# Optimization experiments

Hardware: AMD Instinct MI355X
Metric: run time of the kernel (lower is better)

The kernel has to match this reference:

```python
import jax, jax.numpy as jnp
import numpy as np

N_NODES = 100000
N_EDGES = 640000
IN_DIM, HID_DIM, OUT_DIM = 128, 64, 32


def setup_inputs() -> dict:
    key = jax.random.key(0)
    ks = jax.random.split(key, 8)
    x = jax.random.normal(ks[0], (N_NODES, IN_DIM), dtype=jnp.float32)
    edge_index = jax.random.randint(ks[1], (2, N_EDGES), 0, N_NODES, dtype=jnp.int64)
    # SAGEConv params: lin_l (applied to aggregated neighbors, has bias),
    # lin_r (applied to root node, no bias) -- PyG defaults.
    s1 = 1.0 / np.sqrt(IN_DIM)
    s2 = 1.0 / np.sqrt(HID_DIM)
    W1l = jax.random.uniform(ks[2], (HID_DIM, IN_DIM), jnp.float32, -s1, s1)
    b1 = jax.random.uniform(ks[3], (HID_DIM,), jnp.float32, -s1, s1)
    W1r = jax.random.uniform(ks[4], (HID_DIM, IN_DIM), jnp.float32, -s1, s1)
    W2l = jax.random.uniform(ks[5], (OUT_DIM, HID_DIM), jnp.float32, -s2, s2)
    b2 = jax.random.uniform(ks[6], (OUT_DIM,), jnp.float32, -s2, s2)
    W2r = jax.random.uniform(ks[7], (OUT_DIM, HID_DIM), jnp.float32, -s2, s2)
    return {"x": x, "edge_index": edge_index,
            "W1l": W1l, "b1": b1, "W1r": W1r,
            "W2l": W2l, "b2": b2, "W2r": W2r}


def _sage_conv(x, src, dst, Wl, b, Wr, num_nodes):
    # mean aggregation of source features onto destination nodes
    msg = x[src]                                                # [E, d]
    agg = jax.ops.segment_sum(msg, dst, num_segments=num_nodes)  # [N, d]
    cnt = jax.ops.segment_sum(jnp.ones((src.shape[0],), x.dtype), dst,
                              num_segments=num_nodes)            # [N]
    agg = agg / jnp.maximum(cnt, 1.0)[:, None]
    # out = lin_l(mean_neighbors) + lin_r(x)
    return agg @ Wl.T + b + x @ Wr.T


def reference(x, edge_index, W1l, b1, W1r, W2l, b2, W2r):
    src, dst = edge_index[0], edge_index[1]
    n = x.shape[0]
    h = jax.nn.relu(_sage_conv(x, src, dst, W1l, b1, W1r, n))
    out = _sage_conv(h, src, dst, W2l, b2, W2r, n)
    return out
```

## Files before the change

kernel.cpp:

```cpp
#include <hip/hip_runtime.h>
#include <hip/hip_bf16.h>

typedef __hip_bfloat16 bf16;
typedef __attribute__((ext_vector_type(8))) short short8;
typedef __attribute__((ext_vector_type(4))) float f32x4;

#define N_NODES 100000
#define N_EDGES 640000
#define NSB 98
#define N_TILES 6250
#define GE 313
#define HB 625
#define LIN1_BLKS 1024
#define ECAP 1024

__device__ __forceinline__ float bf2f(short s) {
    union { float f; unsigned u; } u;
    u.u = ((unsigned)(unsigned short)s) << 16;
    return u.f;
}
__device__ __forceinline__ short f2s(float f) {
    union { bf16 b; short s; } u;
    u.b = __float2bfloat16(f);
    return u.s;
}

__device__ __forceinline__ int detect_is64(const int* __restrict__ idx) {
    int lane = threadIdx.x & 63;
    int v = idx[2 * (lane & 31) + 1];
    return __ballot(v == 0) == ~0ULL;
}
__device__ __forceinline__ int detect_f32(const unsigned* __restrict__ xw) {
    int lane = threadIdx.x & 63;
    unsigned e = (xw[lane] >> 7) & 0xFFu;
    int inr = (e >= 0x20u && e <= 0x4Fu);
    return __popcll(__ballot(inr)) < 48;
}

__device__ __forceinline__ void decode8(
        const int* __restrict__ eidx, int is64, int e0, int E,
        int (&ss)[8], int (&dd)[8]) {
    if (is64) {
        int4 a0 = *(const int4*)&eidx[2 * e0];
        int4 a1 = *(const int4*)&eidx[2 * e0 + 4];
        int4 a2 = *(const int4*)&eidx[2 * e0 + 8];
        int4 a3 = *(const int4*)&eidx[2 * e0 + 12];
        int4 b0 = *(const int4*)&eidx[2 * (E + e0)];
        int4 b1 = *(const int4*)&eidx[2 * (E + e0) + 4];
        int4 b2 = *(const int4*)&eidx[2 * (E + e0) + 8];
        int4 b3 = *(const int4*)&eidx[2 * (E + e0) + 12];
        ss[0] = a0.x; ss[1] = a0.z; ss[2] = a1.x; ss[3] = a1.z;
        ss[4] = a2.x; ss[5] = a2.z; ss[6] = a3.x; ss[7] = a3.z;
        dd[0] = b0.x; dd[1] = b0.z; dd[2] = b1.x; dd[3] = b1.z;
        dd[4] = b2.x; dd[5] = b2.z; dd[6] = b3.x; dd[7] = b3.z;
    } else {
        int4 s0 = *(const int4*)&eidx[e0];
        int4 s1 = *(const int4*)&eidx[e0 + 4];
        int4 d0 = *(const int4*)&eidx[E + e0];
        int4 d1 = *(const int4*)&eidx[E + e0 + 4];
        ss[0] = s0.x; ss[1] = s0.y; ss[2] = s0.z; ss[3] = s0.w;
        ss[4] = s1.x; ss[5] = s1.y; ss[6] = s1.z; ss[7] = s1.w;
        dd[0] = d0.x; dd[1] = d0.y; dd[2] = d0.z; dd[3] = d0.w;
        dd[4] = d1.x; dd[5] = d1.y; dd[6] = d1.z; dd[7] = d1.w;
    }
}

__device__ __forceinline__ void decode4(
        const int* __restrict__ eidx, int is64, int e0, int E,
        int (&ss)[4], int (&dd)[4]) {
    if (is64) {
        int4 a0 = *(const int4*)&eidx[2 * e0];
        int4 a1 = *(const int4*)&eidx[2 * e0 + 4];
        int4 b0 = *(const int4*)&eidx[2 * (E + e0)];
        int4 b1 = *(const int4*)&eidx[2 * (E + e0) + 4];
        ss[0] = a0.x; ss[1] = a0.z; ss[2] = a1.x; ss[3] = a1.z;
        dd[0] = b0.x; dd[1] = b0.z; dd[2] = b1.x; dd[3] = b1.z;
    } else {
        int4 s0 = *(const int4*)&eidx[e0];
        int4 d0 = *(const int4*)&eidx[E + e0];
        ss[0] = s0.x; ss[1] = s0.y; ss[2] = s0.z; ss[3] = s0.w;
        dd[0] = d0.x; dd[1] = d0.y; dd[2] = d0.z; dd[3] = d0.w;
    }
}

__global__ __launch_bounds__(256) void hist_kernel(
        const int* __restrict__ eidx, int* __restrict__ deg,
        int* __restrict__ rank) {
    const int is64 = detect_is64(eidx);
    const int e0 = (blockIdx.x * 256 + threadIdx.x) * 4;
    int ss[4], dd[4], rk[4];
    decode4(eidx, is64, e0, N_EDGES, ss, dd);
#pragma unroll
    for (int c = 0; c < 4; ++c) {
        bool ok = (unsigned)ss[c] < (unsigned)N_NODES &&
                  (unsigned)dd[c] < (unsigned)N_NODES;
        rk[c] = ok ? atomicAdd(&deg[dd[c]], 1) : 0;
    }
    *(int4*)&rank[e0] = make_int4(rk[0], rk[1], rk[2], rk[3]);
}

__global__ __launch_bounds__(256) void scan_partial_kernel(
        const int* __restrict__ deg, int* __restrict__ off,
        int* __restrict__ bsum, int N) {
    __shared__ int ss[256];
    const int tid = threadIdx.x, blk = blockIdx.x;
    const int base = blk * 1024 + tid * 4;
    int v[4], s = 0;
    if (base + 3 < N) {
        int4 dv = *(const int4*)&deg[base];
        v[0] = dv.x; v[1] = dv.y; v[2] = dv.z; v[3] = dv.w;
    } else {
#pragma unroll
        for (int c = 0; c < 4; ++c) v[c] = (base + c < N) ? deg[base + c] : 0;
    }
#pragma unroll
    for (int c = 0; c < 4; ++c) s += v[c];
    ss[tid] = s; __syncthreads();
    for (int o = 1; o < 256; o <<= 1) {
        int t = (tid >= o) ? ss[tid - o] : 0;
        __syncthreads();
        ss[tid] += t;
        __syncthreads();
    }
    int run = ss[tid] - s;
    if (tid == 255) bsum[blk] = ss[255];
#pragma unroll
    for (int c = 0; c < 4; ++c) {
        if (base + c < N) off[base + c] = run;
        run += v[c];
    }
}

__global__ __launch_bounds__(256) void scan_add_kernel(
        int* __restrict__ off, const int* __restrict__ bsum, int N) {
    __shared__ int ss[NSB];
    const int blk = blockIdx.x, tid = threadIdx.x;
    if (tid < NSB) ss[tid] = bsum[tid];
    __syncthreads();
    int add = 0;
    for (int i = 0; i < blk; ++i) add += ss[i];
    const int base = blk * 1024 + tid * 4;
#pragma unroll
    for (int c = 0; c < 4; ++c) {
        int i = base + c;
        if (i < N) off[i] += add;
    }
    if (blk == NSB - 1 && tid == 0)
        off[N] = add + ss[NSB - 1];
}

__global__ __launch_bounds__(256) void fill_kernel(
        const int* __restrict__ eidx, const int* __restrict__ off,
        const int* __restrict__ rank, int* __restrict__ srcs, int E, int N) {
    const int is64 = detect_is64(eidx);
    int e0 = (blockIdx.x * 256 + threadIdx.x) * 8;
    if (e0 >= E) return;
    int ss[8], dd[8];
    decode8(eidx, is64, e0, E, ss, dd);
    int4 r0 = *(const int4*)&rank[e0];
    int4 r1 = *(const int4*)&rank[e0 + 4];
    const int rk[8] = {r0.x, r0.y, r0.z, r0.w, r1.x, r1.y, r1.z, r1.w};
#pragma unroll
    for (int c = 0; c < 8; ++c) {
        if ((unsigned)ss[c] >= (unsigned)N || (unsigned)dd[c] >= (unsigned)N) continue;
        srcs[off[dd[c]] + rk[c]] = ss[c];
    }
}

__device__ __forceinline__ short8 load_frag(const void* base, size_t eoff, int f32) {
    if (f32) {
        const float4* p = (const float4*)((const float*)base + eoff);
        const float4 u = p[0], v = p[1];
        short8 r;
        r[0] = f2s(u.x); r[1] = f2s(u.y); r[2] = f2s(u.z); r[3] = f2s(u.w);
        r[4] = f2s(v.x); r[5] = f2s(v.y); r[6] = f2s(v.z); r[7] = f2s(v.w);
        return r;
    }
    return *(const short8*)((const short*)base + eoff);
}

__global__ __launch_bounds__(256) void lin1_kernel(
        const void* __restrict__ x, const void* __restrict__ W1l,
        const void* __restrict__ W1r, bf16* __restrict__ xl,
        bf16* __restrict__ xr) {
    const int f32 = detect_f32((const unsigned*)x);
    __shared__ short wlds[2][16][64][8];

    const int tid = threadIdx.x;
    {
        const int l = tid & 63, fg = tid >> 6;
        const int mm = l & 15, qq = l >> 4;
#pragma unroll
        for (int i = 0; i < 4; ++i) {
            const int f = fg * 4 + i;
            const int ks = f >> 2, dt = f & 3;
            const size_t wo = (size_t)(dt * 16 + mm) * 128 + ks * 32 + qq * 8;
            *(short8*)&wlds[0][f][l][0] = load_frag(W1l, wo, f32);
            *(short8*)&wlds[1][f][l][0] = load_frag(W1r, wo, f32);
        }
    }
    __syncthreads();

    const int nwaves = LIN1_BLKS * 4;
    const int wid = blockIdx.x * 4 + (tid >> 6);
    const int lane = tid & 63;
    const int m = lane & 15, quad = lane >> 4;
    const short* wl0 = &wlds[0][0][lane][0];
    const short* wr0 = &wlds[1][0][lane][0];

    int tile = wid;
    if (tile >= N_TILES) return;

    short8 a[4];
    {
        const size_t arow = (size_t)(tile * 16 + m) * 128 + quad * 8;
#pragma unroll
        for (int ks = 0; ks < 4; ++ks)
            a[ks] = load_frag(x, arow + ks * 32, f32);
    }

    while (true) {
        const int nxt = tile + nwaves;
        short8 an[4];
        if (nxt < N_TILES) {
            const size_t arow = (size_t)(nxt * 16 + m) * 128 + quad * 8;
#pragma unroll
            for (int ks = 0; ks < 4; ++ks)
                an[ks] = load_frag(x, arow + ks * 32, f32);
        }

        f32x4 accl[4], accr[4];
#pragma unroll
        for (int dt = 0; dt < 4; ++dt) {
            accl[dt] = (f32x4){0.f, 0.f, 0.f, 0.f};
            accr[dt] = (f32x4){0.f, 0.f, 0.f, 0.f};
        }
#pragma unroll
        for (int ks = 0; ks < 4; ++ks)
#pragma unroll
            for (int dt = 0; dt < 4; ++dt) {
                const short8 wl = *(const short8*)(wl0 + (ks * 4 + dt) * 512);
                const short8 wr = *(const short8*)(wr0 + (ks * 4 + dt) * 512);
                accl[dt] = __builtin_amdgcn_mfma_f32_16x16x32_bf16(
                    wl, a[ks], accl[dt], 0, 0, 0);
                accr[dt] = __builtin_amdgcn_mfma_f32_16x16x32_bf16(
                    wr, a[ks], accr[dt], 0, 0, 0);
            }

        const int node = tile * 16 + m;
#pragma unroll
        for (int dt = 0; dt < 4; ++dt) {
            short4 pl, pr;
            pl.x = f2s(accl[dt][0]); pl.y = f2s(accl[dt][1]);
            pl.z = f2s(accl[dt][2]); pl.w = f2s(accl[dt][3]);
            pr.x = f2s(accr[dt][0]); pr.y = f2s(accr[dt][1]);
            pr.z = f2s(accr[dt][2]); pr.w = f2s(accr[dt][3]);
            *(short4*)((short*)xl + (size_t)node * 64 + dt * 16 + quad * 4) = pl;
            *(short4*)((short*)xr + (size_t)node * 64 + dt * 16 + quad * 4) = pr;
        }

        if (nxt >= N_TILES) break;
        tile = nxt;
#pragma unroll
        for (int ks = 0; ks < 4; ++ks) a[ks] = an[ks];
    }
}

__global__ __launch_bounds__(256) void gather1_lin2_kernel(
        const int* __restrict__ srcs, const int* __restrict__ off,
        const bf16* __restrict__ xl, const bf16* __restrict__ xr,
        const void* __restrict__ b1, const void* __restrict__ W2l,
        const void* __restrict__ W2r, bf16* __restrict__ hl,
        bf16* __restrict__ hr, const unsigned* __restrict__ xdet) {
    const int f32 = detect_f32(xdet);
    const int tid = threadIdx.x;
    const int lane = tid & 63, wave = tid >> 6;
    const int m = lane & 15, quad = lane >> 4;

    const void* Wb = (wave < 2) ? W2l : W2r;
    short8 bfrag[2];
#pragma unroll
    for (int ks = 0; ks < 2; ++ks)
        bfrag[ks] = load_frag(
            Wb, (size_t)((wave & 1) * 16 + m) * 64 + ks * 32 + quad * 8, f32);

    __shared__ int soff[17];
    __shared__ int slds[ECAP];
    __shared__ short htile[16][72];

    const int n0 = blockIdx.x * 16;
    if (tid < 17) soff[tid] = off[n0 + tid];
    __syncthreads();
    const int base0 = soff[0];
    const int etot = soff[16] - base0;
    for (int i = tid; i < min(etot, ECAP); i += 256) slds[i] = srcs[base0 + i];
    __syncthreads();

    const int g = tid >> 4;
    const int j = tid & 15;
    const int a = soff[g] - base0, b = soff[g + 1] - base0;
    float a0 = 0.f, a1 = 0.f, a2 = 0.f, a3 = 0.f;
    if (etot <= ECAP) {
        for (int e = a; e < b; e += 8) {
            short4 v[8];
#pragma unroll
            for (int t = 0; t < 8; ++t) {
                const int idx = e + t;
                const int s = slds[(idx < b) ? idx : a];
                short4 vv = *(const short4*)((const short*)xl + (size_t)s * 64 + j * 4);
                v[t] = (idx < b) ? vv : make_short4(0, 0, 0, 0);
            }
#pragma unroll
            for (int t = 0; t < 8; ++t) {
                a0 += bf2f(v[t].x); a1 += bf2f(v[t].y);
                a2 += bf2f(v[t].z); a3 += bf2f(v[t].w);
            }
        }
    } else {
        for (int e = a; e < b; ++e) {
            const int s = srcs[base0 + e];
            short4 vv = *(const short4*)((const short*)xl + (size_t)s * 64 + j * 4);
            a0 += bf2f(vv.x); a1 += bf2f(vv.y);
            a2 += bf2f(vv.z); a3 += bf2f(vv.w);
        }
    }
    float b0, b1v, b2v, b3;
    if (f32) {
        float4 bb4 = *(const float4*)((const float*)b1 + j * 4);
        b0 = bb4.x; b1v = bb4.y; b2v = bb4.z; b3 = bb4.w;
    } else {
        short4 bb4 = *(const short4*)((const short*)b1 + j * 4);
        b0 = bf2f(bb4.x); b1v = bf2f(bb4.y); b2v = bf2f(bb4.z); b3 = bf2f(bb4.w);
    }
    const int node = n0 + g;
    short4 xr4 = *(const short4*)((const short*)xr + (size_t)node * 64 + j * 4);
    const float inv = 1.0f / fmaxf((float)(b - a), 1.0f);
    short4 o;
    o.x = f2s(fmaxf(a0 * inv + b0  + bf2f(xr4.x), 0.0f));
    o.y = f2s(fmaxf(a1 * inv + b1v + bf2f(xr4.y), 0.0f));
    o.z = f2s(fmaxf(a2 * inv + b2v + bf2f(xr4.z), 0.0f));
    o.w = f2s(fmaxf(a3 * inv + b3  + bf2f(xr4.w), 0.0f));
    *(short4*)&htile[g][j * 4] = o;
    __syncthreads();

    short8 afr[2];
#pragma unroll
    for (int ks = 0; ks < 2; ++ks)
        afr[ks] = *(const short8*)&htile[m][ks * 32 + quad * 8];
    f32x4 acc = (f32x4){0.f, 0.f, 0.f, 0.f};
#pragma unroll
    for (int ks = 0; ks < 2; ++ks)
        acc = __builtin_amdgcn_mfma_f32_16x16x32_bf16(
            bfrag[ks], afr[ks], acc, 0, 0, 0);

    bf16* dst = (wave < 2) ? hl : hr;
    const int onode = n0 + m;
    short4 p;
    p.x = f2s(acc[0]); p.y = f2s(acc[1]);
    p.z = f2s(acc[2]); p.w = f2s(acc[3]);
    *(short4*)((short*)dst + (size_t)onode * 32 + (wave & 1) * 16 + quad * 4) = p;
}

__global__ __launch_bounds__(256) void gather2_kernel(
        const int* __restrict__ srcs, const int* __restrict__ off,
        const bf16* __restrict__ hl, const bf16* __restrict__ hr,
        const void* __restrict__ b2, void* __restrict__ out,
        const unsigned* __restrict__ xdet, int N) {
    const int f32 = detect_f32(xdet);
    const int tid = threadIdx.x;

    __shared__ int soff[33];
    __shared__ int slds[ECAP];

    const int n0 = blockIdx.x * 32;
    if (tid < 33) soff[tid] = off[n0 + tid];
    __syncthreads();
    const int base0 = soff[0];
    const int etot = soff[32] - base0;
    for (int i = tid; i < min(etot, ECAP); i += 256) slds[i] = srcs[base0 + i];
    __syncthreads();

    const int g = tid >> 3;
    const int j = tid & 7;
    const int a = soff[g] - base0, b = soff[g + 1] - base0;
    float a0 = 0.f, a1 = 0.f, a2 = 0.f, a3 = 0.f;
    if (etot <= ECAP) {
        for (int e = a; e < b; e += 8) {
            short4 v[8];
#pragma unroll
            for (int t = 0; t < 8; ++t) {
                const int idx = e + t;
                const int s = slds[(idx < b) ? idx : a];
                short4 vv = *(const short4*)((const short*)hl + (size_t)s * 32 + j * 4);
                v[t] = (idx < b) ? vv : make_short4(0, 0, 0, 0);
            }
#pragma unroll
            for (int t = 0; t < 8; ++t) {
                a0 += bf2f(v[t].x); a1 += bf2f(v[t].y);
                a2 += bf2f(v[t].z); a3 += bf2f(v[t].w);
            }
        }
    } else {
        for (int e = a; e < b; ++e) {
            const int s = srcs[base0 + e];
            short4 vv = *(const short4*)((const short*)hl + (size_t)s * 32 + j * 4);
            a0 += bf2f(vv.x); a1 += bf2f(vv.y);
            a2 += bf2f(vv.z); a3 += bf2f(vv.w);
        }
    }
    float b0, b1v, b2v, b3;
    if (f32) {
        float4 bb4 = *(const float4*)((const float*)b2 + j * 4);
        b0 = bb4.x; b1v = bb4.y; b2v = bb4.z; b3 = bb4.w;
    } else {
        short4 bb4 = *(const short4*)((const short*)b2 + j * 4);
        b0 = bf2f(bb4.x); b1v = bf2f(bb4.y); b2v = bf2f(bb4.z); b3 = bf2f(bb4.w);
    }
    const int node = n0 + g;
    short4 hr4 = *(const short4*)((const short*)hr + (size_t)node * 32 + j * 4);
    const float inv = 1.0f / fmaxf((float)(b - a), 1.0f);
    const float v0 = a0 * inv + b0  + bf2f(hr4.x);
    const float v1 = a1 * inv + b1v + bf2f(hr4.y);
    const float v2 = a2 * inv + b2v + bf2f(hr4.z);
    const float v3 = a3 * inv + b3  + bf2f(hr4.w);
    if (f32) {
        *(float4*)((float*)out + (size_t)node * 32 + j * 4) =
            make_float4(v0, v1, v2, v3);
    } else {
        short4 o;
        o.x = f2s(v0); o.y = f2s(v1); o.z = f2s(v2); o.w = f2s(v3);
        *(short4*)((short*)out + (size_t)node * 32 + j * 4) = o;
    }
}

extern "C" void kernel_launch(void* const* d_in, const int* in_sizes, int n_in,
                              void* d_out, int out_size, void* d_ws, size_t ws_size,
                              hipStream_t stream) {
    const void* x   = d_in[0];
    const int*  eix = (const int*)d_in[1];
    const void* W1l = d_in[2];
    const void* b1  = d_in[3];
    const void* W1r = d_in[4];
    const void* W2l = d_in[5];
    const void* b2  = d_in[6];
    const void* W2r = d_in[7];

    const int N = N_NODES;
    const int E = N_EDGES;

    char* ws = (char*)d_ws;
    bf16*  xl    = (bf16*)(ws + 256);
    bf16*  xr    = (bf16*)(ws + 256 + (size_t)N * 128);
    bf16*  hl    = (bf16*)(ws + 256 + (size_t)N * 384);
    bf16*  hr    = (bf16*)(ws + 256 + (size_t)N * 448);
    int*   off   = (int*) (ws + 256 + (size_t)N * 512);
    int*   deg   = off + (N + 4);
    int*   rank  = deg + N;
    int*   srcs  = rank + E;
    int*   bsum  = srcs + E;

    hipMemsetAsync(deg, 0, (size_t)N * 4, stream);

    hist_kernel<<<HB, 256, 0, stream>>>(eix, deg, rank);

    scan_partial_kernel<<<NSB, 256, 0, stream>>>(deg, off, bsum, N);
    scan_add_kernel<<<NSB, 256, 0, stream>>>(off, bsum, N);
    fill_kernel<<<GE, 256, 0, stream>>>(eix, off, rank, srcs, E, N);

    lin1_kernel<<<LIN1_BLKS, 256, 0, stream>>>(x, W1l, W1r, xl, xr);

    gather1_lin2_kernel<<<N / 16, 256, 0, stream>>>(
        srcs, off, xl, xr, b1, W2l, W2r, hl, hr, (const unsigned*)x);

    gather2_kernel<<<N / 32, 256, 0, stream>>>(
        srcs, off, hl, hr, b2, d_out, (const unsigned*)x, N);
}
```

Measured before the change: 209.5 us.

## Balance gather work across threads via edge-parallel LDS atomic accumulation

Packs the destination's local row index into the upper bits of each stored source index. Both gather kernels then walk the block's edge list with a flat stride, so every thread group handles the same number of edges. Before, each group looped over its own node's variable-degree neighbor list. Partial sums now go into a shared-memory float tile through LDS atomicAdd, followed by a barrier. This removes per-node degree imbalance and masked padding iterations, but adds four LDS atomics per edge per thread plus zero-initialisation and an extra sync.

```diff
diff --git a/kernel.cpp b/kernel.cpp
--- a/kernel.cpp
+++ b/kernel.cpp
@@ -13,6 +13,7 @@
 #define HB 625
 #define LIN1_BLKS 1024
 #define ECAP 1024
+#define SMASK 0x1FFFF
 
 __device__ __forceinline__ float bf2f(short s) {
     union { float f; unsigned u; } u;
@@ -163,7 +164,7 @@
 #pragma unroll
     for (int c = 0; c < 8; ++c) {
         if ((unsigned)ss[c] >= (unsigned)N || (unsigned)dd[c] >= (unsigned)N) continue;
-        srcs[off[dd[c]] + rk[c]] = ss[c];
+        srcs[off[dd[c]] + rk[c]] = ss[c] | ((dd[c] & 31) << 17);
     }
 }
 
@@ -286,6 +287,7 @@
 
     __shared__ int soff[17];
     __shared__ int slds[ECAP];
+    __shared__ float hacc[16][68];
     __shared__ short htile[16][72];
 
     const int n0 = blockIdx.x * 16;
@@ -294,36 +296,49 @@
     const int base0 = soff[0];
     const int etot = soff[16] - base0;
     for (int i = tid; i < min(etot, ECAP); i += 256) slds[i] = srcs[base0 + i];
+    {
+        float* hf = &hacc[0][0];
+        for (int i = tid; i < 16 * 68; i += 256) hf[i] = 0.f;
+    }
     __syncthreads();
 
     const int g = tid >> 4;
     const int j = tid & 15;
-    const int a = soff[g] - base0, b = soff[g + 1] - base0;
-    float a0 = 0.f, a1 = 0.f, a2 = 0.f, a3 = 0.f;
     if (etot <= ECAP) {
-        for (int e = a; e < b; e += 8) {
-            short4 v[8];
-#pragma unroll
-            for (int t = 0; t < 8; ++t) {
-                const int idx = e + t;
-                const int s = slds[(idx < b) ? idx : a];
-                short4 vv = *(const short4*)((const short*)xl + (size_t)s * 64 + j * 4);
-                v[t] = (idx < b) ? vv : make_short4(0, 0, 0, 0);
+        for (int p = g; p < etot; p += 64) {
+            short4 vv[4]; int gg[4]; bool val[4];
+#pragma unroll
+            for (int t = 0; t < 4; ++t) {
+                const int idx = p + t * 16;
+                val[t] = idx < etot;
+                const int v = slds[val[t] ? idx : p];
+                const int s = v & SMASK;
+                gg[t] = (v >> 17) & 15;
+                vv[t] = *(const short4*)((const short*)xl + (size_t)s * 64 + j * 4);
             }
 #pragma unroll
-            for (int t = 0; t < 8; ++t) {
-                a0 += bf2f(v[t].x); a1 += bf2f(v[t].y);
-                a2 += bf2f(v[t].z); a3 += bf2f(v[t].w);
+            for (int t = 0; t < 4; ++t) {
+                if (!val[t]) continue;
+                atomicAdd(&hacc[gg[t]][j * 4 + 0], bf2f(vv[t].x));
+                atomicAdd(&hacc[gg[t]][j * 4 + 1], bf2f(vv[t].y));
+                atomicAdd(&hacc[gg[t]][j * 4 + 2], bf2f(vv[t].z));
+                atomicAdd(&hacc[gg[t]][j * 4 + 3], bf2f(vv[t].w));
             }
         }
     } else {
+        const int a = soff[g] - base0, b = soff[g + 1] - base0;
+        float a0 = 0.f, a1 = 0.f, a2 = 0.f, a3 = 0.f;
         for (int e = a; e < b; ++e) {
-            const int s = srcs[base0 + e];
+            const int s = srcs[base0 + e] & SMASK;
             short4 vv = *(const short4*)((const short*)xl + (size_t)s * 64 + j * 4);
             a0 += bf2f(vv.x); a1 += bf2f(vv.y);
             a2 += bf2f(vv.z); a3 += bf2f(vv.w);
         }
-    }
+        hacc[g][j * 4 + 0] = a0; hacc[g][j * 4 + 1] = a1;
+        hacc[g][j * 4 + 2] = a2; hacc[g][j * 4 + 3] = a3;
+    }
+    __syncthreads();
+
     float b0, b1v, b2v, b3;
     if (f32) {
         float4 bb4 = *(const float4*)((const float*)b1 + j * 4);
@@ -334,12 +349,12 @@
     }
     const int node = n0 + g;
     short4 xr4 = *(const short4*)((const short*)xr + (size_t)node * 64 + j * 4);
-    const float inv = 1.0f / fmaxf((float)(b - a), 1.0f);
+    const float inv = 1.0f / fmaxf((float)(soff[g + 1] - soff[g]), 1.0f);
     short4 o;
-    o.x = f2s(fmaxf(a0 * inv + b0  + bf2f(xr4.x), 0.0f));
-    o.y = f2s(fmaxf(a1 * inv + b1v + bf2f(xr4.y), 0.0f));
-    o.z = f2s(fmaxf(a2 * inv + b2v + bf2f(xr4.z), 0.0f));
-    o.w = f2s(fmaxf(a3 * inv + b3  + bf2f(xr4.w), 0.0f));
+    o.x = f2s(fmaxf(hacc[g][j * 4 + 0] * inv + b0  + bf2f(xr4.x), 0.0f));
+    o.y = f2s(fmaxf(hacc[g][j * 4 + 1] * inv + b1v + bf2f(xr4.y), 0.0f));
+    o.z = f2s(fmaxf(hacc[g][j * 4 + 2] * inv + b2v + bf2f(xr4.z), 0.0f));
+    o.w = f2s(fmaxf(hacc[g][j * 4 + 3] * inv + b3  + bf2f(xr4.w), 0.0f));
     *(short4*)&htile[g][j * 4] = o;
     __syncthreads();
 
@@ -371,6 +386,7 @@
 
     __shared__ int soff[33];
     __shared__ int slds[ECAP];
+    __shared__ float hacc[32][36];
 
     const int n0 = blockIdx.x * 32;
     if (tid < 33) soff[tid] = off[n0 + tid];
@@ -378,36 +394,49 @@
     const int base0 = soff[0];
     const int etot = soff[32] - base0;
     for (int i = tid; i < min(etot, ECAP); i += 256) slds[i] = srcs[base0 + i];
+    {
+        float* hf = &hacc[0][0];
+        for (int i = tid; i < 32 * 36; i += 256) hf[i] = 0.f;
+    }
     __syncthreads();
 
     const int g = tid >> 3;
     const int j = tid & 7;
-    const int a = soff[g] - base0, b = soff[g + 1] - base0;
-    float a0 = 0.f, a1 = 0.f, a2 = 0.f, a3 = 0.f;
     if (etot <= ECAP) {
-        for (int e = a; e < b; e += 8) {
-            short4 v[8];
-#pragma unroll
-            for (int t = 0; t < 8; ++t) {
-                const int idx = e + t;
-                const int s = slds[(idx < b) ? idx : a];
-                short4 vv = *(const short4*)((const short*)hl + (size_t)s * 32 + j * 4);
-                v[t] = (idx < b) ? vv : make_short4(0, 0, 0, 0);
+        for (int p = g; p < etot; p += 128) {
+            short4 vv[4]; int gg[4]; bool val[4];
+#pragma unroll
+            for (int t = 0; t < 4; ++t) {
+                const int idx = p + t * 32;
+                val[t] = idx < etot;
+                const int v = slds[val[t] ? idx : p];
+                const int s = v & SMASK;
+                gg[t] = (v >> 17) & 31;
+                vv[t] = *(const short4*)((const short*)hl + (size_t)s * 32 + j * 4);
             }
 #pragma unroll
-            for (int t = 0; t < 8; ++t) {
-                a0 += bf2f(v[t].x); a1 += bf2f(v[t].y);
-                a2 += bf2f(v[t].z); a3 += bf2f(v[t].w);
+            for (int t = 0; t < 4; ++t) {
+                if (!val[t]) continue;
+                atomicAdd(&hacc[gg[t]][j * 4 + 0], bf2f(vv[t].x));
+                atomicAdd(&hacc[gg[t]][j * 4 + 1], bf2f(vv[t].y));
+                atomicAdd(&hacc[gg[t]][j * 4 + 2], bf2f(vv[t].z));
+                atomicAdd(&hacc[gg[t]][j * 4 + 3], bf2f(vv[t].w));
             }
         }
     } else {
+        const int a = soff[g] - base0, b = soff[g + 1] - base0;
+        float a0 = 0.f, a1 = 0.f, a2 = 0.f, a3 = 0.f;
         for (int e = a; e < b; ++e) {
-            const int s = srcs[base0 + e];
+            const int s = srcs[base0 + e] & SMASK;
             short4 vv = *(const short4*)((const short*)hl + (size_t)s * 32 + j * 4);
             a0 += bf2f(vv.x); a1 += bf2f(vv.y);
             a2 += bf2f(vv.z); a3 += bf2f(vv.w);
         }
-    }
+        hacc[g][j * 4 + 0] = a0; hacc[g][j * 4 + 1] = a1;
+        hacc[g][j * 4 + 2] = a2; hacc[g][j * 4 + 3] = a3;
+    }
+    __syncthreads();
+
     float b0, b1v, b2v, b3;
     if (f32) {
         float4 bb4 = *(const float4*)((const float*)b2 + j * 4);
@@ -418,11 +447,11 @@
     }
     const int node = n0 + g;
     short4 hr4 = *(const short4*)((const short*)hr + (size_t)node * 32 + j * 4);
-    const float inv = 1.0f / fmaxf((float)(b - a), 1.0f);
-    const float v0 = a0 * inv + b0  + bf2f(hr4.x);
-    const float v1 = a1 * inv + b1v + bf2f(hr4.y);
-    const float v2 = a2 * inv + b2v + bf2f(hr4.z);
-    const float v3 = a3 * inv + b3  + bf2f(hr4.w);
+    const float inv = 1.0f / fmaxf((float)(soff[g + 1] - soff[g]), 1.0f);
+    const float v0 = hacc[g][j * 4 + 0] * inv + b0  + bf2f(hr4.x);
+    const float v1 = hacc[g][j * 4 + 1] * inv + b1v + bf2f(hr4.y);
+    const float v2 = hacc[g][j * 4 + 2] * inv + b2v + bf2f(hr4.z);
+    const float v3 = hacc[g][j * 4 + 3] * inv + b3  + bf2f(hr4.w);
     if (f32) {
         *(float4*)((float*)out + (size_t)node * 32 + j * 4) =
             make_float4(v0, v1, v2, v3);
```

New measurement: 501.6 us. 139% more time.
